# Performance work log

Hardware: AMD Instinct MI355X
Metric: run time of the kernel (lower is better)

The kernel has to match this reference:

```python
import jax, jax.numpy as jnp
import numpy as np

N = 100_000      # total nodes
E = 1_600_000    # total edges
G = 32           # number of graphs in batch
IN = 100         # in_channels
H = 64           # hidden_channels
L = 3            # num_layers
EPS = 1e-5       # BatchNorm eps


def setup_inputs() -> dict:
    key = jax.random.key(0)
    ks = jax.random.split(key, 16)
    x = jax.random.normal(ks[0], (N, IN), jnp.float32)
    edge_index = jax.random.randint(ks[1], (2, E), 0, N)
    edge_weight = jax.random.uniform(ks[2], (E,), jnp.float32)
    batch = jnp.sort(jax.random.randint(ks[3], (N,), 0, G))
    inp = {"x": x, "edge_index": edge_index, "edge_weight": edge_weight, "batch": batch}
    dims = [IN] + [H] * L
    for i in range(L):
        din, dout = dims[i], dims[i + 1]
        s = 1.0 / np.sqrt(din)
        inp[f"W{i}"] = jax.random.uniform(ks[4 + i], (din, dout), jnp.float32, -s, s)
        inp[f"b{i}"] = jnp.zeros((dout,), jnp.float32)
        inp[f"g{i}"] = jnp.ones((dout,), jnp.float32)   # BN gamma
        inp[f"bt{i}"] = jnp.zeros((dout,), jnp.float32)  # BN beta
        inp[f"rm{i}"] = jnp.zeros((dout,), jnp.float32)  # BN running mean
        inp[f"rv{i}"] = jnp.ones((dout,), jnp.float32)   # BN running var
    return inp


def reference(x, edge_index, edge_weight, batch,
              W0, b0, g0, bt0, rm0, rv0,
              W1, b1, g1, bt1, rm1, rv1,
              W2, b2, g2, bt2, rm2, rv2):
    n = x.shape[0]
    loop = jnp.arange(n)
    src = jnp.concatenate([edge_index[0], loop])
    dst = jnp.concatenate([edge_index[1], loop])
    w = jnp.concatenate([jnp.abs(edge_weight), jnp.ones((n,), x.dtype)])
    # symmetric GCN normalization (deg computed on target / col)
    deg = jax.ops.segment_sum(w, dst, num_segments=n)
    deg_safe = jnp.where(deg > 0, deg, 1.0)
    dinv = jnp.where(deg > 0, jax.lax.rsqrt(deg_safe), 0.0)
    norm = dinv[src] * w * dinv[dst]  # [E+N]

    def gcn_bn_relu(h, W, b, g, bt, rm, rv):
        h = h @ W                              # [N, dout]
        msg = h[src] * norm[:, None]           # gather + scale
        h = jax.ops.segment_sum(msg, dst, num_segments=n) + b  # scatter-add
        h = (h - rm) * jax.lax.rsqrt(rv + EPS) * g + bt        # BN (eval)
        return jnp.maximum(h, 0.0)             # ReLU (dropout off in eval)

    h = x
    for (W, b, g, bt, rm, rv) in [(W0, b0, g0, bt0, rm0, rv0),
                                  (W1, b1, g1, bt1, rm1, rv1),
                                  (W2, b2, g2, bt2, rm2, rv2)]:
        h = gcn_bn_relu(h, W, b, g, bt, rm, rv)

    # mean+add global pooling
    s = jax.ops.segment_sum(h, batch, num_segments=G)
    cnt = jax.ops.segment_sum(jnp.ones((n,), h.dtype), batch, num_segments=G)
    mean = s / jnp.maximum(cnt, 1.0)[:, None]
    return jnp.concatenate([mean, s], axis=-1)  # [G, 2*H]
```

## Files before the change

### kernel.cpp

```cpp
#include <hip/hip_runtime.h>
#include <hip/hip_bf16.h>

#define NN 100000
#define EE 1600000
#define GG 32
#define INC 100
#define HC 64
#define CAP 64
#define BN_EPS 1e-5f
#define NB_POOL 1563
#define WQ 32767.0f
#define NSLICE 8
#define SLICE_N 12500
#define EBLK 6250

typedef __hip_bfloat16 bf16;

__device__ __forceinline__ float bflo(unsigned u) { return __uint_as_float(u << 16); }
__device__ __forceinline__ float bfhi(unsigned u) { return __uint_as_float(u & 0xffff0000u); }
__device__ __forceinline__ unsigned f2bf(float f) {
    unsigned x = __float_as_uint(f);
    return (x + 0x7fffu + ((x >> 16) & 1u)) >> 16;
}
__device__ __forceinline__ unsigned bfpack(float lo, float hi) {
    return f2bf(lo) | (f2bf(hi) << 16);
}


__global__ __launch_bounds__(256) void k_scatter_ell(const int* __restrict__ ei,
                                                     const float* __restrict__ ew,
                                                     int* __restrict__ cur,
                                                     unsigned* __restrict__ epk) {
    unsigned b = blockIdx.x;
    int slice = b & (NSLICE - 1);
    int e = (int)(b >> 3) * 256 + threadIdx.x;
    if (e >= EE) return;
    int d = __builtin_nontemporal_load(&ei[EE + e]);
    int lo = slice * SLICE_N;
    if (d < lo || d >= lo + SLICE_N) return;
    int s = __builtin_nontemporal_load(&ei[e]);
    float w = __builtin_nontemporal_load(&ew[e]);
    int qw = (int)(fabsf(w) * WQ + 0.5f);
    if (qw > 32767) qw = 32767;
    int slot = atomicAdd(&cur[d], 1);
    if (slot < CAP)
        epk[(size_t)d * CAP + slot] = ((unsigned)s << 15) | (unsigned)qw;
}

__global__ __launch_bounds__(256) void k_dinv_ell(const int* __restrict__ cur,
                                                  const unsigned* __restrict__ epk,
                                                  float* __restrict__ dinv) {
    int wid = (blockIdx.x * 256 + threadIdx.x) >> 6;
    int lane = threadIdx.x & 63;
    if (wid >= NN) return;
    int cnt = min(cur[wid], CAP);
    float v = 0.f;
    if (lane < cnt)
        v = (float)(epk[(size_t)wid * CAP + lane] & 0x7fffu) * (1.0f / WQ);
    for (int o = 32; o > 0; o >>= 1) v += __shfl_down(v, o);
    if (lane == 0) dinv[wid] = rsqrtf(v + 1.0f);
}

__global__ void k_norm_ell(const int* __restrict__ cur, unsigned* __restrict__ epk,
                           const float* __restrict__ dinv) {
    int idx = blockIdx.x * 256 + threadIdx.x;
    if (idx >= NN * CAP) return;
    int d = idx >> 6, slot = idx & (CAP - 1);
    if (slot >= min(cur[d], CAP)) return;
    unsigned k = epk[idx];
    int s = k >> 15;
    float c = dinv[s] * (float)(k & 0x7fffu) * (1.0f / WQ) * dinv[d];
    int q = (int)(c * WQ + 0.5f);
    if (q > 32767) q = 32767;
    epk[idx] = (k & 0xffff8000u) | (unsigned)q;
}


__device__ __forceinline__ float ldf(const float* p, size_t i) { return p[i]; }
__device__ __forceinline__ float ldf(const bf16* p, size_t i) { return __bfloat162float(p[i]); }

template <int DIN, typename Tin>
__global__ __launch_bounds__(256) void k_gemm(const Tin* __restrict__ X,
                                              const float* __restrict__ W,
                                              bf16* __restrict__ Y) {
    __shared__ float Ws[DIN * 64];
    __shared__ float Xs[32 * DIN];
    int row0 = blockIdx.x * 32;
    for (int idx = threadIdx.x; idx < DIN * 64; idx += 256)
        Ws[idx] = W[idx];
    for (int idx = threadIdx.x; idx < 32 * DIN; idx += 256) {
        int r = idx / DIN, k = idx - r * DIN;
        Xs[idx] = ldf(X, (size_t)(row0 + r) * DIN + k);
    }
    __syncthreads();
    int c = threadIdx.x & 63;
    int r0 = threadIdx.x >> 6;
    float acc[8];
#pragma unroll
    for (int j = 0; j < 8; j++) acc[j] = 0.f;
    for (int k = 0; k < DIN; k++) {
        float wv = Ws[k * 64 + c];
#pragma unroll
        for (int j = 0; j < 8; j++)
            acc[j] += Xs[(r0 + j * 4) * DIN + k] * wv;
    }
#pragma unroll
    for (int j = 0; j < 8; j++)
        Y[(size_t)(row0 + r0 + j * 4) * 64 + c] = __float2bfloat16(acc[j]);
}


__global__ __launch_bounds__(256) void k_gather_bn(
    const unsigned* __restrict__ hw32, const int* __restrict__ cur,
    const unsigned* __restrict__ epk, const float* __restrict__ dinv,
    const float* __restrict__ bb, const float* __restrict__ gg,
    const float* __restrict__ btp, const float* __restrict__ rmp,
    const float* __restrict__ rvp, unsigned* __restrict__ ho32) {
    int wave = (blockIdx.x * 256 + threadIdx.x) >> 6;
    int lane = threadIdx.x & 63;
    int n = wave * 2 + (lane >> 5);
    int l5 = lane & 31;
    if (n >= NN) return;
    float di = dinv[n];
    float d2 = di * di;
    unsigned us = hw32[(size_t)n * 32 + l5];
    float a0 = bflo(us) * d2, b0 = bfhi(us) * d2;
    float a1 = 0.f, b1 = 0.f, a2 = 0.f, b2 = 0.f;
    float a3 = 0.f, b3 = 0.f, a4 = 0.f, b4 = 0.f;
    int cnt = min(cur[n], CAP);
    const unsigned* ce = epk + (size_t)n * CAP;
    const float q = 1.0f / WQ;
    unsigned klo = (l5 < cnt) ? ce[l5] : 0u;
    unsigned khi = 0u;
    if (cnt > 32) khi = (32 + l5 < cnt) ? ce[32 + l5] : 0u;
    int p = 0;
    for (; p + 8 <= cnt; p += 8) {
        unsigned base = (p < 32) ? klo : khi;
        int pb = p & 31;
        unsigned k0 = __shfl(base, pb + 0, 32);
        unsigned k1 = __shfl(base, pb + 1, 32);
        unsigned k2 = __shfl(base, pb + 2, 32);
        unsigned k3 = __shfl(base, pb + 3, 32);
        unsigned k4 = __shfl(base, pb + 4, 32);
        unsigned k5 = __shfl(base, pb + 5, 32);
        unsigned k6 = __shfl(base, pb + 6, 32);
        unsigned k7 = __shfl(base, pb + 7, 32);
        unsigned u0 = hw32[(size_t)(k0 >> 15) * 32 + l5];
        unsigned u1 = hw32[(size_t)(k1 >> 15) * 32 + l5];
        unsigned u2 = hw32[(size_t)(k2 >> 15) * 32 + l5];
        unsigned u3 = hw32[(size_t)(k3 >> 15) * 32 + l5];
        unsigned u4 = hw32[(size_t)(k4 >> 15) * 32 + l5];
        unsigned u5 = hw32[(size_t)(k5 >> 15) * 32 + l5];
        unsigned u6 = hw32[(size_t)(k6 >> 15) * 32 + l5];
        unsigned u7 = hw32[(size_t)(k7 >> 15) * 32 + l5];
        float c0 = (float)(k0 & 0x7fffu) * q, c1 = (float)(k1 & 0x7fffu) * q;
        float c2 = (float)(k2 & 0x7fffu) * q, c3 = (float)(k3 & 0x7fffu) * q;
        float c4 = (float)(k4 & 0x7fffu) * q, c5 = (float)(k5 & 0x7fffu) * q;
        float c6 = (float)(k6 & 0x7fffu) * q, c7 = (float)(k7 & 0x7fffu) * q;
        a0 += bflo(u0) * c0; b0 += bfhi(u0) * c0;
        a1 += bflo(u1) * c1; b1 += bfhi(u1) * c1;
        a2 += bflo(u2) * c2; b2 += bfhi(u2) * c2;
        a3 += bflo(u3) * c3; b3 += bfhi(u3) * c3;
        a4 += bflo(u4) * c4; b4 += bfhi(u4) * c4;
        a0 += bflo(u5) * c5; b0 += bfhi(u5) * c5;
        a1 += bflo(u6) * c6; b1 += bfhi(u6) * c6;
        a2 += bflo(u7) * c7; b2 += bfhi(u7) * c7;
    }
    for (; p + 4 <= cnt; p += 4) {
        unsigned base = (p < 32) ? klo : khi;
        int pb = p & 31;
        unsigned k0 = __shfl(base, pb + 0, 32);
        unsigned k1 = __shfl(base, pb + 1, 32);
        unsigned k2 = __shfl(base, pb + 2, 32);
        unsigned k3 = __shfl(base, pb + 3, 32);
        unsigned u0 = hw32[(size_t)(k0 >> 15) * 32 + l5];
        unsigned u1 = hw32[(size_t)(k1 >> 15) * 32 + l5];
        unsigned u2 = hw32[(size_t)(k2 >> 15) * 32 + l5];
        unsigned u3 = hw32[(size_t)(k3 >> 15) * 32 + l5];
        float c0 = (float)(k0 & 0x7fffu) * q, c1 = (float)(k1 & 0x7fffu) * q;
        float c2 = (float)(k2 & 0x7fffu) * q, c3 = (float)(k3 & 0x7fffu) * q;
        a0 += bflo(u0) * c0; b0 += bfhi(u0) * c0;
        a1 += bflo(u1) * c1; b1 += bfhi(u1) * c1;
        a2 += bflo(u2) * c2; b2 += bfhi(u2) * c2;
        a3 += bflo(u3) * c3; b3 += bfhi(u3) * c3;
    }
    for (; p < cnt; ++p) {
        unsigned base = (p < 32) ? klo : khi;
        unsigned k0 = __shfl(base, p & 31, 32);
        unsigned u0 = hw32[(size_t)(k0 >> 15) * 32 + l5];
        float c0 = (float)(k0 & 0x7fffu) * q;
        a0 += bflo(u0) * c0; b0 += bfhi(u0) * c0;
    }
    int cl = l5 * 2, ch = cl + 1;
    float alo = ((a0 + a1) + (a2 + a3)) + a4 + bb[cl];
    float ahi = ((b0 + b1) + (b2 + b3)) + b4 + bb[ch];
    float slo = gg[cl] * rsqrtf(rvp[cl] + BN_EPS);
    float shi = gg[ch] * rsqrtf(rvp[ch] + BN_EPS);
    float olo = fmaxf((alo - rmp[cl]) * slo + btp[cl], 0.f);
    float ohi = fmaxf((ahi - rmp[ch]) * shi + btp[ch], 0.f);
    ho32[(size_t)n * 32 + l5] = bfpack(olo, ohi);
}


__global__ __launch_bounds__(64) void k_pool(const bf16* __restrict__ h,
                                             const int* __restrict__ batch,
                                             float* __restrict__ s, float* __restrict__ cntf) {
    int c = threadIdx.x;
    int n0 = blockIdx.x * 64;
    if (n0 >= NN) return;
    int n1 = n0 + 64; if (n1 > NN) n1 = NN;
    float acc = 0.f, cnt = 0.f;
    int gcur = batch[n0];
    for (int i = n0; i < n1; ++i) {
        int gi = batch[i];
        if (gi != gcur) {
            atomicAdd(&s[gcur * 64 + c], acc);
            if (c == 0) atomicAdd(&cntf[gcur], cnt);
            acc = 0.f; cnt = 0.f; gcur = gi;
        }
        acc += __bfloat162float(h[(size_t)i * 64 + c]);
        cnt += 1.f;
    }
    atomicAdd(&s[gcur * 64 + c], acc);
    if (c == 0) atomicAdd(&cntf[gcur], cnt);
}


__global__ void k_out(const float* __restrict__ s, const float* __restrict__ cntf,
                      float* __restrict__ out) {
    int idx = blockIdx.x * 256 + threadIdx.x;
    if (idx >= GG * 128) return;
    int g = idx >> 7, c = idx & 127;
    float v;
    if (c < 64) v = s[g * 64 + c] / fmaxf(cntf[g], 1.f);
    else        v = s[g * 64 + (c - 64)];
    out[idx] = v;
}


extern "C" void kernel_launch(void* const* d_in, const int* in_sizes, int n_in,
                              void* d_out, int out_size, void* d_ws, size_t ws_size,
                              hipStream_t stream) {
    const float* x   = (const float*)d_in[0];
    const int* ei    = (const int*)d_in[1];
    const float* ew  = (const float*)d_in[2];
    const int* batch = (const int*)d_in[3];
    const float *Wp[3], *bp[3], *gp[3], *btp[3], *rmp[3], *rvp[3];
    for (int l = 0; l < 3; ++l) {
        Wp[l]  = (const float*)d_in[4 + 6 * l + 0];
        bp[l]  = (const float*)d_in[4 + 6 * l + 1];
        gp[l]  = (const float*)d_in[4 + 6 * l + 2];
        btp[l] = (const float*)d_in[4 + 6 * l + 3];
        rmp[l] = (const float*)d_in[4 + 6 * l + 4];
        rvp[l] = (const float*)d_in[4 + 6 * l + 5];
    }

    size_t off = 0;
    auto carve = [&](size_t bytes) {
        void* r = (char*)d_ws + off;
        off += (bytes + 255) & ~(size_t)255;
        return r;
    };
    int*      cur    = (int*)     carve(NN * 4);
    float*    dinv   = (float*)   carve(NN * 4);
    unsigned* epk    = (unsigned*)carve((size_t)NN * CAP * 4);
    bf16*     hw     = (bf16*)    carve((size_t)NN * 64 * 2);
    bf16*     ha     = (bf16*)    carve((size_t)NN * 64 * 2);
    float*    pool_s = (float*)   carve(GG * 64 * 4);
    float*    pool_c = (float*)   carve(GG * 4);

    hipMemsetAsync(cur, 0, NN * 4, stream);
    hipMemsetAsync(pool_s, 0, GG * 64 * 4, stream);
    hipMemsetAsync(pool_c, 0, GG * 4, stream);

    int nwblk  = (NN * 64 + 255) / 256;
    int gatblk = NN / 8;
    int gemm_grid = NN / 32;

    k_scatter_ell<<<EBLK * NSLICE, 256, 0, stream>>>(ei, ew, cur, epk);
    k_dinv_ell<<<nwblk, 256, 0, stream>>>(cur, epk, dinv);
    k_norm_ell<<<nwblk, 256, 0, stream>>>(cur, epk, dinv);

    k_gemm<INC, float><<<gemm_grid, 256, 0, stream>>>(x, Wp[0], hw);
    k_gather_bn<<<gatblk, 256, 0, stream>>>((unsigned*)hw, cur, epk, dinv,
                                            bp[0], gp[0], btp[0], rmp[0], rvp[0], (unsigned*)ha);
    k_gemm<HC, bf16><<<gemm_grid, 256, 0, stream>>>(ha, Wp[1], hw);
    k_gather_bn<<<gatblk, 256, 0, stream>>>((unsigned*)hw, cur, epk, dinv,
                                            bp[1], gp[1], btp[1], rmp[1], rvp[1], (unsigned*)ha);
    k_gemm<HC, bf16><<<gemm_grid, 256, 0, stream>>>(ha, Wp[2], hw);
    k_gather_bn<<<gatblk, 256, 0, stream>>>((unsigned*)hw, cur, epk, dinv,
                                            bp[2], gp[2], btp[2], rmp[2], rvp[2], (unsigned*)ha);

    k_pool<<<NB_POOL, 64, 0, stream>>>(ha, batch, pool_s, pool_c);
    k_out<<<(GG * 128 + 255) / 256, 256, 0, stream>>>(pool_s, pool_c, (float*)d_out);
}
```

Measured before the change: 482.5 us.

## Fold symmetric norm into GEMM scaling and fuse gather with next-layer GEMM

Drops the k_norm_ell pass. Edge coefficients now stay as raw quantized weights, and the source-side dinv is applied in the GEMM epilogue while the destination-side dinv is applied after aggregation. Layers 1 and 2 merge the gather/BN/ReLU with the following 64x64 GEMM: results go through shared memory, so the intermediate bf16 activation is no longer written to and re-read from global memory. The cost is loading the weight matrix into shared memory in every 8-node block and an extra block barrier. Quantization error also changes, since raw weights are quantized instead of normalized coefficients.

```diff
diff --git a/kernel.cpp b/kernel.cpp
--- a/kernel.cpp
+++ b/kernel.cpp
@@ -61,20 +61,6 @@
     if (lane == 0) dinv[wid] = rsqrtf(v + 1.0f);
 }
 
-__global__ void k_norm_ell(const int* __restrict__ cur, unsigned* __restrict__ epk,
-                           const float* __restrict__ dinv) {
-    int idx = blockIdx.x * 256 + threadIdx.x;
-    if (idx >= NN * CAP) return;
-    int d = idx >> 6, slot = idx & (CAP - 1);
-    if (slot >= min(cur[d], CAP)) return;
-    unsigned k = epk[idx];
-    int s = k >> 15;
-    float c = dinv[s] * (float)(k & 0x7fffu) * (1.0f / WQ) * dinv[d];
-    int q = (int)(c * WQ + 0.5f);
-    if (q > 32767) q = 32767;
-    epk[idx] = (k & 0xffff8000u) | (unsigned)q;
-}
-
 
 __device__ __forceinline__ float ldf(const float* p, size_t i) { return p[i]; }
 __device__ __forceinline__ float ldf(const bf16* p, size_t i) { return __bfloat162float(p[i]); }
@@ -82,6 +68,7 @@
 template <int DIN, typename Tin>
 __global__ __launch_bounds__(256) void k_gemm(const Tin* __restrict__ X,
                                               const float* __restrict__ W,
+                                              const float* __restrict__ dinv,
                                               bf16* __restrict__ Y) {
     __shared__ float Ws[DIN * 64];
     __shared__ float Xs[32 * DIN];
@@ -105,8 +92,121 @@
             acc[j] += Xs[(r0 + j * 4) * DIN + k] * wv;
     }
 #pragma unroll
-    for (int j = 0; j < 8; j++)
-        Y[(size_t)(row0 + r0 + j * 4) * 64 + c] = __float2bfloat16(acc[j]);
+    for (int j = 0; j < 8; j++) {
+        int row = row0 + r0 + j * 4;
+        Y[(size_t)row * 64 + c] = __float2bfloat16(acc[j] * dinv[row]);
+    }
+}
+
+
+__global__ __launch_bounds__(256) void k_gather_gemm(
+    const unsigned* __restrict__ hw32, const int* __restrict__ cur,
+    const unsigned* __restrict__ epk, const float* __restrict__ dinv,
+    const float* __restrict__ bb, const float* __restrict__ gg,
+    const float* __restrict__ btp, const float* __restrict__ rmp,
+    const float* __restrict__ rvp, const float* __restrict__ W,
+    unsigned* __restrict__ out32) {
+    __shared__ float Ws[64 * 64];
+    __shared__ float hs[8][64];
+    int tid = threadIdx.x;
+    for (int idx = tid; idx < 64 * 64; idx += 256)
+        Ws[idx] = W[idx];
+
+    int lane = tid & 63;
+    int l5 = lane & 31;
+    int local = (tid >> 6) * 2 + (lane >> 5);
+    int n = blockIdx.x * 8 + local;
+    float di = dinv[n];
+    unsigned us = hw32[(size_t)n * 32 + l5];
+    float a0 = bflo(us), b0 = bfhi(us);
+    float a1 = 0.f, b1 = 0.f, a2 = 0.f, b2 = 0.f;
+    float a3 = 0.f, b3 = 0.f, a4 = 0.f, b4 = 0.f;
+    int cnt = min(cur[n], CAP);
+    const unsigned* ce = epk + (size_t)n * CAP;
+    const float q = 1.0f / WQ;
+    unsigned klo = (l5 < cnt) ? ce[l5] : 0u;
+    unsigned khi = 0u;
+    if (cnt > 32) khi = (32 + l5 < cnt) ? ce[32 + l5] : 0u;
+    int p = 0;
+    for (; p + 8 <= cnt; p += 8) {
+        unsigned base = (p < 32) ? klo : khi;
+        int pb = p & 31;
+        unsigned k0 = __shfl(base, pb + 0, 32);
+        unsigned k1 = __shfl(base, pb + 1, 32);
+        unsigned k2 = __shfl(base, pb + 2, 32);
+        unsigned k3 = __shfl(base, pb + 3, 32);
+        unsigned k4 = __shfl(base, pb + 4, 32);
+        unsigned k5 = __shfl(base, pb + 5, 32);
+        unsigned k6 = __shfl(base, pb + 6, 32);
+        unsigned k7 = __shfl(base, pb + 7, 32);
+        unsigned u0 = hw32[(size_t)(k0 >> 15) * 32 + l5];
+        unsigned u1 = hw32[(size_t)(k1 >> 15) * 32 + l5];
+        unsigned u2 = hw32[(size_t)(k2 >> 15) * 32 + l5];
+        unsigned u3 = hw32[(size_t)(k3 >> 15) * 32 + l5];
+        unsigned u4 = hw32[(size_t)(k4 >> 15) * 32 + l5];
+        unsigned u5 = hw32[(size_t)(k5 >> 15) * 32 + l5];
+        unsigned u6 = hw32[(size_t)(k6 >> 15) * 32 + l5];
+        unsigned u7 = hw32[(size_t)(k7 >> 15) * 32 + l5];
+        float c0 = (float)(k0 & 0x7fffu) * q, c1 = (float)(k1 & 0x7fffu) * q;
+        float c2 = (float)(k2 & 0x7fffu) * q, c3 = (float)(k3 & 0x7fffu) * q;
+        float c4 = (float)(k4 & 0x7fffu) * q, c5 = (float)(k5 & 0x7fffu) * q;
+        float c6 = (float)(k6 & 0x7fffu) * q, c7 = (float)(k7 & 0x7fffu) * q;
+        a0 += bflo(u0) * c0; b0 += bfhi(u0) * c0;
+        a1 += bflo(u1) * c1; b1 += bfhi(u1) * c1;
+        a2 += bflo(u2) * c2; b2 += bfhi(u2) * c2;
+        a3 += bflo(u3) * c3; b3 += bfhi(u3) * c3;
+        a4 += bflo(u4) * c4; b4 += bfhi(u4) * c4;
+        a0 += bflo(u5) * c5; b0 += bfhi(u5) * c5;
+        a1 += bflo(u6) * c6; b1 += bfhi(u6) * c6;
+        a2 += bflo(u7) * c7; b2 += bfhi(u7) * c7;
+    }
+    for (; p + 4 <= cnt; p += 4) {
+        unsigned base = (p < 32) ? klo : khi;
+        int pb = p & 31;
+        unsigned k0 = __shfl(base, pb + 0, 32);
+        unsigned k1 = __shfl(base, pb + 1, 32);
+        unsigned k2 = __shfl(base, pb + 2, 32);
+        unsigned k3 = __shfl(base, pb + 3, 32);
+        unsigned u0 = hw32[(size_t)(k0 >> 15) * 32 + l5];
+        unsigned u1 = hw32[(size_t)(k1 >> 15) * 32 + l5];
+        unsigned u2 = hw32[(size_t)(k2 >> 15) * 32 + l5];
+        unsigned u3 = hw32[(size_t)(k3 >> 15) * 32 + l5];
+        float c0 = (float)(k0 & 0x7fffu) * q, c1 = (float)(k1 & 0x7fffu) * q;
+        float c2 = (float)(k2 & 0x7fffu) * q, c3 = (float)(k3 & 0x7fffu) * q;
+        a0 += bflo(u0) * c0; b0 += bfhi(u0) * c0;
+        a1 += bflo(u1) * c1; b1 += bfhi(u1) * c1;
+        a2 += bflo(u2) * c2; b2 += bfhi(u2) * c2;
+        a3 += bflo(u3) * c3; b3 += bfhi(u3) * c3;
+    }
+    for (; p < cnt; ++p) {
+        unsigned base = (p < 32) ? klo : khi;
+        unsigned k0 = __shfl(base, p & 31, 32);
+        unsigned u0 = hw32[(size_t)(k0 >> 15) * 32 + l5];
+        float c0 = (float)(k0 & 0x7fffu) * q;
+        a0 += bflo(u0) * c0; b0 += bfhi(u0) * c0;
+    }
+    int cl = l5 * 2, ch = cl + 1;
+    float alo = (((a0 + a1) + (a2 + a3)) + a4) * di + bb[cl];
+    float ahi = (((b0 + b1) + (b2 + b3)) + b4) * di + bb[ch];
+    float slo = gg[cl] * rsqrtf(rvp[cl] + BN_EPS);
+    float shi = gg[ch] * rsqrtf(rvp[ch] + BN_EPS);
+    hs[local][cl] = fmaxf((alo - rmp[cl]) * slo + btp[cl], 0.f);
+    hs[local][ch] = fmaxf((ahi - rmp[ch]) * shi + btp[ch], 0.f);
+    __syncthreads();
+
+    int r = tid >> 5;
+    int pr = tid & 31;
+    int c2 = pr * 2;
+    float accl = 0.f, acch = 0.f;
+#pragma unroll 8
+    for (int k = 0; k < 64; ++k) {
+        float h = hs[r][k];
+        accl += h * Ws[k * 64 + c2];
+        acch += h * Ws[k * 64 + c2 + 1];
+    }
+    int rn = blockIdx.x * 8 + r;
+    float dib = dinv[rn];
+    out32[(size_t)rn * 32 + pr] = bfpack(accl * dib, acch * dib);
 }
 
 
@@ -122,9 +222,8 @@
     int l5 = lane & 31;
     if (n >= NN) return;
     float di = dinv[n];
-    float d2 = di * di;
     unsigned us = hw32[(size_t)n * 32 + l5];
-    float a0 = bflo(us) * d2, b0 = bfhi(us) * d2;
+    float a0 = bflo(us), b0 = bfhi(us);
     float a1 = 0.f, b1 = 0.f, a2 = 0.f, b2 = 0.f;
     float a3 = 0.f, b3 = 0.f, a4 = 0.f, b4 = 0.f;
     int cnt = min(cur[n], CAP);
@@ -192,8 +291,8 @@
         a0 += bflo(u0) * c0; b0 += bfhi(u0) * c0;
     }
     int cl = l5 * 2, ch = cl + 1;
-    float alo = ((a0 + a1) + (a2 + a3)) + a4 + bb[cl];
-    float ahi = ((b0 + b1) + (b2 + b3)) + b4 + bb[ch];
+    float alo = (((a0 + a1) + (a2 + a3)) + a4) * di + bb[cl];
+    float ahi = (((b0 + b1) + (b2 + b3)) + b4) * di + bb[ch];
     float slo = gg[cl] * rsqrtf(rvp[cl] + BN_EPS);
     float shi = gg[ch] * rsqrtf(rvp[ch] + BN_EPS);
     float olo = fmaxf((alo - rmp[cl]) * slo + btp[cl], 0.f);
@@ -279,15 +378,14 @@
 
     k_scatter_ell<<<EBLK * NSLICE, 256, 0, stream>>>(ei, ew, cur, epk);
     k_dinv_ell<<<nwblk, 256, 0, stream>>>(cur, epk, dinv);
-    k_norm_ell<<<nwblk, 256, 0, stream>>>(cur, epk, dinv);
-
-    k_gemm<INC, float><<<gemm_grid, 256, 0, stream>>>(x, Wp[0], hw);
-    k_gather_bn<<<gatblk, 256, 0, stream>>>((unsigned*)hw, cur, epk, dinv,
-                                            bp[0], gp[0], btp[0], rmp[0], rvp[0], (unsigned*)ha);
-    k_gemm<HC, bf16><<<gemm_grid, 256, 0, stream>>>(ha, Wp[1], hw);
-    k_gather_bn<<<gatblk, 256, 0, stream>>>((unsigned*)hw, cur, epk, dinv,
-                                            bp[1], gp[1], btp[1], rmp[1], rvp[1], (unsigned*)ha);
-    k_gemm<HC, bf16><<<gemm_grid, 256, 0, stream>>>(ha, Wp[2], hw);
+
+    k_gemm<INC, float><<<gemm_grid, 256, 0, stream>>>(x, Wp[0], dinv, hw);
+    k_gather_gemm<<<gatblk, 256, 0, stream>>>((unsigned*)hw, cur, epk, dinv,
+                                              bp[0], gp[0], btp[0], rmp[0], rvp[0],
+                                              Wp[1], (unsigned*)ha);
+    k_gather_gemm<<<gatblk, 256, 0, stream>>>((unsigned*)ha, cur, epk, dinv,
+                                              bp[1], gp[1], btp[1], rmp[1], rvp[1],
+                                              Wp[2], (unsigned*)hw);
     k_gather_bn<<<gatblk, 256, 0, stream>>>((unsigned*)hw, cur, epk, dinv,
                                             bp[2], gp[2], btp[2], rmp[2], rvp[2], (unsigned*)ha);
 
```

After: 468.2 us. 1.03x faster.
